# Kernel tuning notes

Measured on AMD Instinct MI355X. Metric: run time of the kernel, lower is better.

The kernel has to match this reference:

```python
import jax, jax.numpy as jnp
import numpy as np

DIM = 1024
HID = 2048
E = 4

def setup_inputs() -> dict:
    key = jax.random.key(0)
    ks = jax.random.split(key, 7)
    s = lambda fan_in: 1.0 / np.sqrt(fan_in)
    x = jax.random.normal(ks[0], (2, 2048, DIM), dtype=jnp.float32)
    W1 = jax.random.uniform(ks[1], (E, DIM, HID), jnp.float32, -s(DIM), s(DIM))
    b1 = jax.random.uniform(ks[2], (E, HID), jnp.float32, -s(DIM), s(DIM))
    W2 = jax.random.uniform(ks[3], (E, HID, DIM), jnp.float32, -s(HID), s(HID))
    b2 = jax.random.uniform(ks[4], (E, DIM), jnp.float32, -s(HID), s(HID))
    Wr = jax.random.uniform(ks[5], (DIM, E), jnp.float32, -s(DIM), s(DIM))
    br = jax.random.uniform(ks[6], (E,), jnp.float32, -s(DIM), s(DIM))
    return {"x": x, "W1": W1, "b1": b1, "W2": W2, "b2": b2, "Wr": Wr, "br": br}

def reference(x, W1, b1, W2, b2, Wr, br):
    # router softmax weights: [B,T,E]
    weights = jax.nn.softmax(x @ Wr + br, axis=-1)
    # all-expert MLP: hidden [B,T,E,H]
    h = jax.nn.gelu(jnp.einsum('btd,edh->bteh', x, W1) + b1, approximate=False)
    # expert outputs [B,T,E,D]
    y = jnp.einsum('bteh,ehd->bted', h, W2) + b2
    # softmax-weighted combine over experts
    return jnp.einsum('bte,bted->btd', weights, y)
```

## Files before the change

### kernel.cpp

```cpp
#include <hip/hip_runtime.h>
#include <hip/hip_bf16.h>
#include <math.h>

#define DIM 1024
#define HID 2048
#define NE  4
#define NT  4096
#define KW  (NE*HID)
#define KSPLIT 4
#define KCH (KW / KSPLIT)

typedef __attribute__((ext_vector_type(8))) short short8;
typedef __attribute__((ext_vector_type(4))) short short4v;
typedef __attribute__((ext_vector_type(4))) float floatx4;


__device__ __forceinline__ void async_cp16(const void* g, void* l) {
  __builtin_amdgcn_global_load_lds(
      (const __attribute__((address_space(1))) void*)g,
      (__attribute__((address_space(3))) void*)l, 16, 0, 0);
}

__device__ __forceinline__ short f2bf(float f) {
  union { float f; unsigned u; } x; x.f = f;
  unsigned r = x.u + 0x7fffu + ((x.u >> 16) & 1u);
  return (short)(r >> 16);
}

__device__ __forceinline__ float gelu_fast(float v) {
  float u = 1.595769122f * (v + 0.044715f * v * v * v);
  return v * __builtin_amdgcn_rcpf(1.0f + __expf(-u));
}

__global__ void router_cvt(const float* __restrict__ x, const float* __restrict__ Wr,
                           const float* __restrict__ br, float* __restrict__ wgt,
                           short* __restrict__ xb) {
  const int wv = threadIdx.x >> 6, lane = threadIdx.x & 63;
  const int t = blockIdx.x * 4 + wv;
  const float* xr = x + (size_t)t * DIM;
  short* xo = xb + (size_t)t * DIM;
  float a0 = 0.f, a1 = 0.f, a2 = 0.f, a3 = 0.f;
  #pragma unroll
  for (int p = 0; p < 4; p++) {
    const int d = p * 256 + lane * 4;
    floatx4 v = *(const floatx4*)&xr[d];
    short4v o;
    #pragma unroll
    for (int j = 0; j < 4; j++) {
      o[j] = f2bf(v[j]);
      floatx4 wr = *(const floatx4*)&Wr[(d + j) * 4];
      a0 += v[j] * wr[0]; a1 += v[j] * wr[1];
      a2 += v[j] * wr[2]; a3 += v[j] * wr[3];
    }
    *(short4v*)&xo[d] = o;
  }
  #pragma unroll
  for (int off = 32; off; off >>= 1) {
    a0 += __shfl_down(a0, off);
    a1 += __shfl_down(a1, off);
    a2 += __shfl_down(a2, off);
    a3 += __shfl_down(a3, off);
  }
  a0 = __shfl(a0, 0); a1 = __shfl(a1, 0); a2 = __shfl(a2, 0); a3 = __shfl(a3, 0);
  float s0 = a0 + br[0], s1 = a1 + br[1], s2 = a2 + br[2], s3 = a3 + br[3];
  float m = fmaxf(fmaxf(s0, s1), fmaxf(s2, s3));
  float e0 = __expf(s0 - m), e1 = __expf(s1 - m), e2 = __expf(s2 - m), e3 = __expf(s3 - m);
  float inv = 1.f / (e0 + e1 + e2 + e3);
  float v = (lane == 0) ? e0 : (lane == 1) ? e1 : (lane == 2) ? e2 : e3;
  if (lane < 4) wgt[t * 4 + lane] = v * inv;
}

#define TP_PADR 136
__global__ void transpose_cvt_fast(const float* __restrict__ in, short* __restrict__ out,
                                   int R, int C) {
  __shared__ __align__(16) short tile[32 * TP_PADR];
  const size_t zo = (size_t)blockIdx.z * (size_t)R * C;
  const int c0 = blockIdx.x * 32, r0 = blockIdx.y * 128;
  const int t = threadIdx.x;
  const int cin = (t & 7) * 4;
  const int rin = t >> 3;
  #pragma unroll
  for (int i = 0; i < 4; i++) {
    const int r = rin + i * 32;
    floatx4 v = *(const floatx4*)&in[zo + (size_t)(r0 + r) * C + c0 + cin];
    #pragma unroll
    for (int j = 0; j < 4; j++)
      tile[(cin + j) * TP_PADR + r] = f2bf(v[j]);
  }
  __syncthreads();
  const int ct = t >> 3;
  #pragma unroll
  for (int i = 0; i < 2; i++) {
    const int rc = (t & 7) + 8 * i;
    short8 vv = *(const short8*)&tile[ct * TP_PADR + rc * 8];
    *(short8*)&out[zo + (size_t)(c0 + ct) * R + r0 + rc * 8] = vv;
  }
}

__global__ void bias_init(const float* __restrict__ wgt, const float* __restrict__ b2,
                          float* __restrict__ out) {
  const int i = (blockIdx.x * 256 + threadIdx.x) * 4;
  const int t = i >> 10, d = i & (DIM - 1);
  floatx4 w = *(const floatx4*)&wgt[t * 4];
  floatx4 r = (floatx4)0.f;
  #pragma unroll
  for (int e = 0; e < 4; e++) {
    floatx4 bv = *(const floatx4*)&b2[e * DIM + d];
    r += w[e] * bv;
  }
  *(floatx4*)&out[i] = r;
}


__global__ __launch_bounds__(256, 2)
void gemm1_kernel(const short* __restrict__ xb, const short* __restrict__ w1t,
                  const float* __restrict__ b1, const float* __restrict__ wgt,
                  short* __restrict__ hw) {
  const int e  = blockIdx.z;
  const int m0 = blockIdx.y * 128;
  const int n0 = blockIdx.x * 128;
  const int tid = threadIdx.x;
  const int lane = tid & 63;
  const int wv = tid >> 6;
  const int wm = (wv >> 1) * 64, wn = (wv & 1) * 64;
  const int quad = lane >> 4, lrow = lane & 15;
  const int sr  = tid >> 3;
  const int kof = ((tid & 7) ^ (sr & 7)) * 8;
  const int rkey = lrow & 7;

  __shared__ __align__(16) short As[128 * 64];
  __shared__ __align__(16) short Bs[128 * 64];

  const short* Ap = xb;
  const short* Bp = w1t + (size_t)e * HID * DIM;

  floatx4 acc[4][4];
  #pragma unroll
  for (int i = 0; i < 4; i++)
    #pragma unroll
    for (int j = 0; j < 4; j++) acc[i][j] = (floatx4)0.f;

  for (int k0 = 0; k0 < DIM; k0 += 64) {
    __syncthreads();
    #pragma unroll
    for (int c = 0; c < 4; c++)
      async_cp16(Ap + (size_t)(m0 + c * 32 + sr) * DIM + k0 + kof,
                 As + (c * 256 + tid) * 8);
    #pragma unroll
    for (int c = 0; c < 4; c++)
      async_cp16(Bp + (size_t)(n0 + c * 32 + sr) * DIM + k0 + kof,
                 Bs + (c * 256 + tid) * 8);
    __syncthreads();
    #pragma unroll
    for (int kk = 0; kk < 2; kk++) {
      short8 af[4], bf[4];
      const int ko = ((kk * 4 + quad) ^ rkey) * 8;
      #pragma unroll
      for (int i = 0; i < 4; i++)
        af[i] = *(const short8*)&As[(wm + i * 16 + lrow) * 64 + ko];
      #pragma unroll
      for (int j = 0; j < 4; j++)
        bf[j] = *(const short8*)&Bs[(wn + j * 16 + lrow) * 64 + ko];
      #pragma unroll
      for (int i = 0; i < 4; i++)
        #pragma unroll
        for (int j = 0; j < 4; j++)
          acc[i][j] = __builtin_amdgcn_mfma_f32_16x16x32_bf16(af[i], bf[j], acc[i][j], 0, 0, 0);
    }
  }

  #pragma unroll
  for (int i = 0; i < 4; i++) {
    const int rbase = m0 + wm + i * 16 + quad * 4;
    float wv4[4];
    #pragma unroll
    for (int r = 0; r < 4; r++) wv4[r] = wgt[(rbase + r) * NE + e];
    #pragma unroll
    for (int j = 0; j < 4; j++) {
      const int col = n0 + wn + j * 16 + lrow;
      const float b = b1[e * HID + col];
      #pragma unroll
      for (int r = 0; r < 4; r++) {
        float v = acc[i][j][r] + b;
        hw[(size_t)(rbase + r) * KW + e * HID + col] = f2bf(wv4[r] * gelu_fast(v));
      }
    }
  }
}

__global__ __launch_bounds__(256, 2)
void gemm2_kernel(const short* __restrict__ hw, const short* __restrict__ w2t,
                  float* __restrict__ out) {
  const int kz = blockIdx.z;
  const int m0 = blockIdx.y * 128;
  const int n0 = blockIdx.x * 128;
  const int tid = threadIdx.x;
  const int lane = tid & 63;
  const int wv = tid >> 6;
  const int wm = (wv >> 1) * 64, wn = (wv & 1) * 64;
  const int quad = lane >> 4, lrow = lane & 15;
  const int sr  = tid >> 3;
  const int kof = ((tid & 7) ^ (sr & 7)) * 8;
  const int rkey = lrow & 7;

  __shared__ __align__(16) short As[128 * 64];
  __shared__ __align__(16) short Bs[128 * 64];

  floatx4 acc[4][4];
  #pragma unroll
  for (int i = 0; i < 4; i++)
    #pragma unroll
    for (int j = 0; j < 4; j++) acc[i][j] = (floatx4)0.f;

  const int kbeg = kz * KCH;
  for (int kk0 = 0; kk0 < KCH; kk0 += 64) {
    const int k0 = kbeg + kk0;
    __syncthreads();
    #pragma unroll
    for (int c = 0; c < 4; c++)
      async_cp16(hw + (size_t)(m0 + c * 32 + sr) * KW + k0 + kof,
                 As + (c * 256 + tid) * 8);
    #pragma unroll
    for (int c = 0; c < 4; c++)
      async_cp16(w2t + (size_t)(n0 + c * 32 + sr) * KW + k0 + kof,
                 Bs + (c * 256 + tid) * 8);
    __syncthreads();
    #pragma unroll
    for (int kk = 0; kk < 2; kk++) {
      short8 af[4], bf[4];
      const int ko = ((kk * 4 + quad) ^ rkey) * 8;
      #pragma unroll
      for (int i = 0; i < 4; i++)
        af[i] = *(const short8*)&As[(wm + i * 16 + lrow) * 64 + ko];
      #pragma unroll
      for (int j = 0; j < 4; j++)
        bf[j] = *(const short8*)&Bs[(wn + j * 16 + lrow) * 64 + ko];
      #pragma unroll
      for (int i = 0; i < 4; i++)
        #pragma unroll
        for (int j = 0; j < 4; j++)
          acc[i][j] = __builtin_amdgcn_mfma_f32_16x16x32_bf16(af[i], bf[j], acc[i][j], 0, 0, 0);
    }
  }

  #pragma unroll
  for (int i = 0; i < 4; i++) {
    const int rbase = m0 + wm + i * 16 + quad * 4;
    #pragma unroll
    for (int j = 0; j < 4; j++) {
      const int col = n0 + wn + j * 16 + lrow;
      #pragma unroll
      for (int r = 0; r < 4; r++)
        atomicAdd(&out[(size_t)(rbase + r) * DIM + col], acc[i][j][r]);
    }
  }
}


extern "C" void kernel_launch(void* const* d_in, const int* in_sizes, int n_in,
                              void* d_out, int out_size, void* d_ws, size_t ws_size,
                              hipStream_t stream) {
  const float* x  = (const float*)d_in[0];
  const float* W1 = (const float*)d_in[1];
  const float* b1 = (const float*)d_in[2];
  const float* W2 = (const float*)d_in[3];
  const float* b2 = (const float*)d_in[4];
  const float* Wr = (const float*)d_in[5];
  const float* br = (const float*)d_in[6];
  float* out = (float*)d_out;

  char* ws = (char*)d_ws;
  float* wgt = (float*)(ws);
  short* w2t = (short*)(ws + 65536);
  short* hw  = (short*)(ws + 65536 + 16777216);
  short* xb  = (short*)(ws + 65536 + 16777216 + 67108864);
  short* w1t = (short*)(ws + 65536 + 16777216 + 67108864 + 8388608);

  hipLaunchKernelGGL(router_cvt, dim3(NT / 4), dim3(256), 0, stream, x, Wr, br, wgt, xb);
  hipLaunchKernelGGL(transpose_cvt_fast, dim3(HID / 32, DIM / 128, NE), dim3(256), 0, stream,
                     W1, w1t, DIM, HID);
  hipLaunchKernelGGL(transpose_cvt_fast, dim3(DIM / 32, KW / 128, 1), dim3(256), 0, stream,
                     W2, w2t, KW, DIM);
  hipLaunchKernelGGL(bias_init, dim3(NT * DIM / 1024), dim3(256), 0, stream, wgt, b2, out);
  hipLaunchKernelGGL(gemm1_kernel, dim3(HID / 128, NT / 128, NE), dim3(256), 0, stream,
                     xb, w1t, b1, wgt, hw);
  hipLaunchKernelGGL(gemm2_kernel, dim3(DIM / 128, NT / 128, KSPLIT), dim3(256), 0, stream,
                     hw, w2t, out);
}
```

Measured before the change: 329.3 us.

## Replace split-K atomics with partial buffers and a reduce kernel; merge transposes

Result: faster. 307.6 us (-6.6%).

```diff
diff --git a/kernel.cpp b/kernel.cpp
--- a/kernel.cpp
+++ b/kernel.cpp
@@ -71,18 +71,28 @@
 }
 
 #define TP_PADR 136
-__global__ void transpose_cvt_fast(const float* __restrict__ in, short* __restrict__ out,
-                                   int R, int C) {
+__global__ void transpose_all(const float* __restrict__ W1, short* __restrict__ w1t,
+                              const float* __restrict__ W2, short* __restrict__ w2t) {
   __shared__ __align__(16) short tile[32 * TP_PADR];
-  const size_t zo = (size_t)blockIdx.z * (size_t)R * C;
-  const int c0 = blockIdx.x * 32, r0 = blockIdx.y * 128;
+  const int b = blockIdx.x;
+  const float* in; short* out; int R, C, xt, yt;
+  if (b < 2048) {
+    const int e = b >> 9, rem = b & 511;
+    xt = rem & 63; yt = rem >> 6; R = DIM; C = HID;
+    in = W1 + (size_t)e * DIM * HID; out = w1t + (size_t)e * DIM * HID;
+  } else {
+    const int rem = b - 2048;
+    xt = rem & 31; yt = rem >> 5; R = KW; C = DIM;
+    in = W2; out = w2t;
+  }
+  const int c0 = xt * 32, r0 = yt * 128;
   const int t = threadIdx.x;
   const int cin = (t & 7) * 4;
   const int rin = t >> 3;
   #pragma unroll
   for (int i = 0; i < 4; i++) {
     const int r = rin + i * 32;
-    floatx4 v = *(const floatx4*)&in[zo + (size_t)(r0 + r) * C + c0 + cin];
+    floatx4 v = *(const floatx4*)&in[(size_t)(r0 + r) * C + c0 + cin];
     #pragma unroll
     for (int j = 0; j < 4; j++)
       tile[(cin + j) * TP_PADR + r] = f2bf(v[j]);
@@ -93,22 +103,8 @@
   for (int i = 0; i < 2; i++) {
     const int rc = (t & 7) + 8 * i;
     short8 vv = *(const short8*)&tile[ct * TP_PADR + rc * 8];
-    *(short8*)&out[zo + (size_t)(c0 + ct) * R + r0 + rc * 8] = vv;
-  }
-}
-
-__global__ void bias_init(const float* __restrict__ wgt, const float* __restrict__ b2,
-                          float* __restrict__ out) {
-  const int i = (blockIdx.x * 256 + threadIdx.x) * 4;
-  const int t = i >> 10, d = i & (DIM - 1);
-  floatx4 w = *(const floatx4*)&wgt[t * 4];
-  floatx4 r = (floatx4)0.f;
-  #pragma unroll
-  for (int e = 0; e < 4; e++) {
-    floatx4 bv = *(const floatx4*)&b2[e * DIM + d];
-    r += w[e] * bv;
-  }
-  *(floatx4*)&out[i] = r;
+    *(short8*)&out[(size_t)(c0 + ct) * R + r0 + rc * 8] = vv;
+  }
 }
 
 
@@ -190,7 +186,8 @@
 
 __global__ __launch_bounds__(256, 2)
 void gemm2_kernel(const short* __restrict__ hw, const short* __restrict__ w2t,
-                  float* __restrict__ out) {
+                  const float* __restrict__ b2, const float* __restrict__ wgt,
+                  float* __restrict__ out, float* __restrict__ part) {
   const int kz = blockIdx.z;
   const int m0 = blockIdx.y * 128;
   const int n0 = blockIdx.x * 128;
@@ -243,17 +240,51 @@
     }
   }
 
-  #pragma unroll
-  for (int i = 0; i < 4; i++) {
-    const int rbase = m0 + wm + i * 16 + quad * 4;
-    #pragma unroll
-    for (int j = 0; j < 4; j++) {
-      const int col = n0 + wn + j * 16 + lrow;
-      #pragma unroll
-      for (int r = 0; r < 4; r++)
-        atomicAdd(&out[(size_t)(rbase + r) * DIM + col], acc[i][j][r]);
-    }
-  }
+  if (kz == 0) {
+    #pragma unroll
+    for (int i = 0; i < 4; i++) {
+      const int rbase = m0 + wm + i * 16 + quad * 4;
+      floatx4 wr[4];
+      #pragma unroll
+      for (int r = 0; r < 4; r++) wr[r] = *(const floatx4*)&wgt[(rbase + r) * NE];
+      #pragma unroll
+      for (int j = 0; j < 4; j++) {
+        const int col = n0 + wn + j * 16 + lrow;
+        float b2v[4];
+        #pragma unroll
+        for (int eI = 0; eI < 4; eI++) b2v[eI] = b2[eI * DIM + col];
+        #pragma unroll
+        for (int r = 0; r < 4; r++) {
+          float bias = wr[r][0] * b2v[0] + wr[r][1] * b2v[1] +
+                       wr[r][2] * b2v[2] + wr[r][3] * b2v[3];
+          out[(size_t)(rbase + r) * DIM + col] = acc[i][j][r] + bias;
+        }
+      }
+    }
+  } else {
+    float* p = part + (size_t)(kz - 1) * NT * DIM;
+    #pragma unroll
+    for (int i = 0; i < 4; i++) {
+      const int rbase = m0 + wm + i * 16 + quad * 4;
+      #pragma unroll
+      for (int j = 0; j < 4; j++) {
+        const int col = n0 + wn + j * 16 + lrow;
+        #pragma unroll
+        for (int r = 0; r < 4; r++)
+          p[(size_t)(rbase + r) * DIM + col] = acc[i][j][r];
+      }
+    }
+  }
+}
+
+__global__ void reduce_out(float* __restrict__ out, const float* __restrict__ part) {
+  int i = (blockIdx.x * 256 + threadIdx.x) * 4;
+  floatx4 v = *(const floatx4*)&out[i];
+  floatx4 a = *(const floatx4*)&part[i];
+  floatx4 b = *(const floatx4*)&part[i + NT * DIM];
+  floatx4 c = *(const floatx4*)&part[i + 2 * NT * DIM];
+  v = v + a + b + c;
+  *(floatx4*)&out[i] = v;
 }
 
 
@@ -275,15 +306,14 @@
   short* hw  = (short*)(ws + 65536 + 16777216);
   short* xb  = (short*)(ws + 65536 + 16777216 + 67108864);
   short* w1t = (short*)(ws + 65536 + 16777216 + 67108864 + 8388608);
+  float* part= (float*)(ws + 65536 + 16777216 + 67108864);
 
   hipLaunchKernelGGL(router_cvt, dim3(NT / 4), dim3(256), 0, stream, x, Wr, br, wgt, xb);
-  hipLaunchKernelGGL(transpose_cvt_fast, dim3(HID / 32, DIM / 128, NE), dim3(256), 0, stream,
-                     W1, w1t, DIM, HID);
-  hipLaunchKernelGGL(transpose_cvt_fast, dim3(DIM / 32, KW / 128, 1), dim3(256), 0, stream,
-                     W2, w2t, KW, DIM);
-  hipLaunchKernelGGL(bias_init, dim3(NT * DIM / 1024), dim3(256), 0, stream, wgt, b2, out);
+  hipLaunchKernelGGL(transpose_all, dim3(2048 + 2048), dim3(256), 0, stream,
+                     W1, w1t, W2, w2t);
   hipLaunchKernelGGL(gemm1_kernel, dim3(HID / 128, NT / 128, NE), dim3(256), 0, stream,
                      xb, w1t, b1, wgt, hw);
   hipLaunchKernelGGL(gemm2_kernel, dim3(DIM / 128, NT / 128, KSPLIT), dim3(256), 0, stream,
-                     hw, w2t, out);
-}
+                     hw, w2t, b2, wgt, out, part);
+  hipLaunchKernelGGL(reduce_out, dim3(NT * DIM / 1024), dim3(256), 0, stream, out, part);
+}
```
